# Kernel optimization log

Measured on AMD Instinct MI355X. Metric: run time of the kernel, lower is better.

## Reference

```python
import jax, jax.numpy as jnp
import numpy as np

M, K, D = 8, 4096, 512  # groups, codes per group, total dim
DG = D // M             # per-group dim = 64


def setup_inputs() -> dict:
    key = jax.random.key(0)
    k1, k2, k3 = jax.random.split(key, 3)
    codes = jax.random.randint(k1, (32, 64, 64, M), 0, K, dtype=jnp.int32)
    codebook = jax.random.normal(k2, (M, K, DG), dtype=jnp.float32)
    wv = jax.random.normal(k3, (M, DG, DG), dtype=jnp.float32) / np.sqrt(DG)
    return {"codes": codes, "codebook": codebook, "wv": wv}


def reference(codes, codebook, wv):
    # v[m,k,c] = sum_d codebook[m,k,d] * wv[m,c,d]  (small per-group GEMM)
    v = jnp.einsum('mkd,mcd->mkc', codebook, wv)  # [M, K, DG]
    # one-hot matmul over k is exactly an indexed gather:
    # gathered[n,h,w,m,c] = v[m, codes[n,h,w,m], c]
    m_idx = jnp.arange(v.shape[0])  # [M]
    gathered = v[m_idx[None, None, None, :], codes]  # [n,h,w,M,DG]
    n, h, w = codes.shape[:3]
    out = gathered.reshape(n, h, w, -1)          # [n,h,w,D]
    return jnp.transpose(out, (0, 3, 1, 2))      # [n,D,h,w]
```

## Files before the change

### kernel.cpp

```cpp
#include <hip/hip_runtime.h>

#define MQ 8
#define KQ 4096
#define DG 64
#define NN 32
#define HW 4096
#define DD 512

typedef float f32x4 __attribute__((ext_vector_type(4)));

__global__ __launch_bounds__(256) void compute_v_kernel(
    const float* __restrict__ codebook,
    const float* __restrict__ wv,
    float* __restrict__ v) {
  __shared__ float wv_t[DG][DG + 1];
  __shared__ float cb[64][DG];

  const int m = blockIdx.y;
  const int k0 = blockIdx.x * 64;
  const int tid = threadIdx.x;

  const float4* wvm4 = (const float4*)(wv + (size_t)m * DG * DG);
  for (int i = tid; i < DG * DG / 4; i += 256) {
    int c = i >> 4, d4 = (i & 15) * 4;
    float4 val = wvm4[i];
    wv_t[d4 + 0][c] = val.x;
    wv_t[d4 + 1][c] = val.y;
    wv_t[d4 + 2][c] = val.z;
    wv_t[d4 + 3][c] = val.w;
  }
  const float4* cbm4 = (const float4*)(codebook + ((size_t)m * KQ + k0) * DG);
  float4* cb4 = (float4*)&cb[0][0];
  for (int i = tid; i < 64 * DG / 4; i += 256) cb4[i] = cbm4[i];
  __syncthreads();

  const int c = tid & 63;
  const int kq = tid >> 6;

  float acc[16];
#pragma unroll
  for (int kl = 0; kl < 16; ++kl) acc[kl] = 0.f;

  for (int d4 = 0; d4 < DG; d4 += 4) {
    float w0 = wv_t[d4 + 0][c];
    float w1 = wv_t[d4 + 1][c];
    float w2 = wv_t[d4 + 2][c];
    float w3 = wv_t[d4 + 3][c];
#pragma unroll
    for (int kl = 0; kl < 16; ++kl) {
      float4 cbv = *(const float4*)&cb[kq * 16 + kl][d4];
      acc[kl] += cbv.x * w0 + cbv.y * w1 + cbv.z * w2 + cbv.w * w3;
    }
  }

  float* vout = v + ((size_t)(m * 16 + (c >> 2)) * KQ) * 4 + (c & 3);
#pragma unroll
  for (int kl = 0; kl < 16; ++kl) {
    vout[(size_t)(k0 + kq * 16 + kl) * 4] = acc[kl];
  }
}

__global__ __launch_bounds__(512, 4) void gather_lut_kernel(
    const int* __restrict__ codes,
    const float* __restrict__ v,
    float* __restrict__ out) {
  __shared__ f32x4 lut[KQ];

  const int b = blockIdx.x;
  const int m = b & 7;
  const int rest = b >> 3;
  const int cq = rest & 15;
  const int n0 = (rest >> 4) * 4;

  const int tid = threadIdx.x;
  const int w = tid >> 6;
  const int l = tid & 63;

  int rr[32];
#pragma unroll
  for (int i = 0; i < 4; ++i) {
    const int* cp = codes + (size_t)(n0 + i) * HW * MQ + m;
#pragma unroll
    for (int q = 0; q < 2; ++q) {
      const int hwb = (w * 2 + q) * 256 + 4 * l;
#pragma unroll
      for (int t = 0; t < 4; ++t)
        rr[i * 8 + q * 4 + t] = cp[(size_t)(hwb + t) * MQ];
    }
  }

  const f32x4* vq = (const f32x4*)(v + (size_t)(m * 16 + cq) * KQ * 4);
#pragma unroll
  for (int i = 0; i < 8; ++i) {
    int k = i * 512 + tid;
    lut[k] = vq[k];
  }
  __syncthreads();

#pragma unroll
  for (int i = 0; i < 4; ++i) {
    float* ob = out + ((size_t)(n0 + i) * DD + m * DG + cq * 4) * HW;
#pragma unroll
    for (int q = 0; q < 2; ++q) {
      const int hwb = (w * 2 + q) * 256 + 4 * l;
      f32x4 v0 = lut[rr[i * 8 + q * 4 + 0]];
      f32x4 v1 = lut[rr[i * 8 + q * 4 + 1]];
      f32x4 v2 = lut[rr[i * 8 + q * 4 + 2]];
      f32x4 v3 = lut[rr[i * 8 + q * 4 + 3]];
      f32x4 o0 = {v0.x, v1.x, v2.x, v3.x};
      f32x4 o1 = {v0.y, v1.y, v2.y, v3.y};
      f32x4 o2 = {v0.z, v1.z, v2.z, v3.z};
      f32x4 o3 = {v0.w, v1.w, v2.w, v3.w};
      __builtin_nontemporal_store(o0, (f32x4*)(ob + 0 * HW + hwb));
      __builtin_nontemporal_store(o1, (f32x4*)(ob + 1 * HW + hwb));
      __builtin_nontemporal_store(o2, (f32x4*)(ob + 2 * HW + hwb));
      __builtin_nontemporal_store(o3, (f32x4*)(ob + 3 * HW + hwb));
    }
  }
}

extern "C" void kernel_launch(void* const* d_in, const int* in_sizes, int n_in,
                              void* d_out, int out_size, void* d_ws, size_t ws_size,
                              hipStream_t stream) {
  const int* codes = (const int*)d_in[0];
  const float* codebook = (const float*)d_in[1];
  const float* wv = (const float*)d_in[2];
  float* out = (float*)d_out;
  float* v = (float*)d_ws;

  compute_v_kernel<<<dim3(64, 8), 256, 0, stream>>>(codebook, wv, v);
  gather_lut_kernel<<<MQ * 16 * (NN / 4), 512, 0, stream>>>(codes, v, out);
}
```

Baseline: 320.9 us.

## Gather directly from global v instead of staging per-plane LUT in LDS

```diff
diff --git a/kernel.cpp b/kernel.cpp
--- a/kernel.cpp
+++ b/kernel.cpp
@@ -60,62 +60,43 @@
   }
 }
 
-__global__ __launch_bounds__(512, 4) void gather_lut_kernel(
+__global__ __launch_bounds__(256, 4) void gather_direct_kernel(
     const int* __restrict__ codes,
     const float* __restrict__ v,
     float* __restrict__ out) {
-  __shared__ f32x4 lut[KQ];
-
   const int b = blockIdx.x;
   const int m = b & 7;
-  const int rest = b >> 3;
-  const int cq = rest & 15;
-  const int n0 = (rest >> 4) * 4;
+  const int chunk = (b >> 3) & 3;
+  const int n = b >> 5;
 
   const int tid = threadIdx.x;
-  const int w = tid >> 6;
-  const int l = tid & 63;
+  const int hw0 = chunk * 1024 + 4 * tid;
 
-  int rr[32];
-#pragma unroll
-  for (int i = 0; i < 4; ++i) {
-    const int* cp = codes + (size_t)(n0 + i) * HW * MQ + m;
-#pragma unroll
-    for (int q = 0; q < 2; ++q) {
-      const int hwb = (w * 2 + q) * 256 + 4 * l;
-#pragma unroll
-      for (int t = 0; t < 4; ++t)
-        rr[i * 8 + q * 4 + t] = cp[(size_t)(hwb + t) * MQ];
-    }
-  }
+  const int* cp = codes + ((size_t)n * HW + hw0) * MQ + m;
+  const int r0 = cp[0 * MQ];
+  const int r1 = cp[1 * MQ];
+  const int r2 = cp[2 * MQ];
+  const int r3 = cp[3 * MQ];
 
-  const f32x4* vq = (const f32x4*)(v + (size_t)(m * 16 + cq) * KQ * 4);
-#pragma unroll
-  for (int i = 0; i < 8; ++i) {
-    int k = i * 512 + tid;
-    lut[k] = vq[k];
-  }
-  __syncthreads();
+  const f32x4* vq = (const f32x4*)v + (size_t)m * 16 * KQ;
+  float* ob = out + ((size_t)n * DD + m * DG) * HW + hw0;
 
 #pragma unroll
-  for (int i = 0; i < 4; ++i) {
-    float* ob = out + ((size_t)(n0 + i) * DD + m * DG + cq * 4) * HW;
-#pragma unroll
-    for (int q = 0; q < 2; ++q) {
-      const int hwb = (w * 2 + q) * 256 + 4 * l;
-      f32x4 v0 = lut[rr[i * 8 + q * 4 + 0]];
-      f32x4 v1 = lut[rr[i * 8 + q * 4 + 1]];
-      f32x4 v2 = lut[rr[i * 8 + q * 4 + 2]];
-      f32x4 v3 = lut[rr[i * 8 + q * 4 + 3]];
-      f32x4 o0 = {v0.x, v1.x, v2.x, v3.x};
-      f32x4 o1 = {v0.y, v1.y, v2.y, v3.y};
-      f32x4 o2 = {v0.z, v1.z, v2.z, v3.z};
-      f32x4 o3 = {v0.w, v1.w, v2.w, v3.w};
-      __builtin_nontemporal_store(o0, (f32x4*)(ob + 0 * HW + hwb));
-      __builtin_nontemporal_store(o1, (f32x4*)(ob + 1 * HW + hwb));
-      __builtin_nontemporal_store(o2, (f32x4*)(ob + 2 * HW + hwb));
-      __builtin_nontemporal_store(o3, (f32x4*)(ob + 3 * HW + hwb));
-    }
+  for (int cq = 0; cq < 16; ++cq) {
+    const f32x4* plane = vq + (size_t)cq * KQ;
+    f32x4 v0 = plane[r0];
+    f32x4 v1 = plane[r1];
+    f32x4 v2 = plane[r2];
+    f32x4 v3 = plane[r3];
+    f32x4 o0 = {v0.x, v1.x, v2.x, v3.x};
+    f32x4 o1 = {v0.y, v1.y, v2.y, v3.y};
+    f32x4 o2 = {v0.z, v1.z, v2.z, v3.z};
+    f32x4 o3 = {v0.w, v1.w, v2.w, v3.w};
+    float* oc = ob + (size_t)(cq * 4) * HW;
+    __builtin_nontemporal_store(o0, (f32x4*)(oc + 0 * HW));
+    __builtin_nontemporal_store(o1, (f32x4*)(oc + 1 * HW));
+    __builtin_nontemporal_store(o2, (f32x4*)(oc + 2 * HW));
+    __builtin_nontemporal_store(o3, (f32x4*)(oc + 3 * HW));
   }
 }
 
@@ -129,5 +110,5 @@
   float* v = (float*)d_ws;
 
   compute_v_kernel<<<dim3(64, 8), 256, 0, stream>>>(codebook, wv, v);
-  gather_lut_kernel<<<MQ * 16 * (NN / 4), 512, 0, stream>>>(codes, v, out);
+  gather_direct_kernel<<<NN * 4 * MQ, 256, 0, stream>>>(codes, v, out);
 }
```

Measured after the change: 305.4 us. 4.8% less time.
